# Performance work log

Measured on AMD Instinct MI355X. Metric: run time of the kernel, lower is better.

## Reference

```python
import jax, jax.numpy as jnp
import numpy as np

BS, SL, D, H = 8, 1024, 1024, 16
DK = D // H


def setup_inputs() -> dict:
    key = jax.random.key(0)
    ks = jax.random.split(key, 12)
    mk = lambda k, shape, s=1.0: jax.random.normal(k, shape, dtype=jnp.float32) * s
    return {
        "q": mk(ks[0], (BS, SL, D)),
        "k": mk(ks[1], (BS, SL, D)),
        "v": mk(ks[2], (BS, SL, D)),
        "mask": jax.random.randint(ks[3], (BS, SL), 0, 2, dtype=jnp.int32),
        "wq": mk(ks[4], (D, D), 0.02), "bq": jnp.zeros((D,), jnp.float32),
        "wk": mk(ks[5], (D, D), 0.02), "bk": jnp.zeros((D,), jnp.float32),
        "wv": mk(ks[6], (D, D), 0.02), "bv": jnp.zeros((D,), jnp.float32),
        "wo": mk(ks[7], (D, D), 0.02), "bo": jnp.zeros((D,), jnp.float32),
    }


def reference(q, k, v, mask, wq, bq, wk, bk, wv, bv, wo, bo):
    bs, sl, d = q.shape
    # linear projections (torch Linear: x @ W^T + b), split heads -> [b, h, s, dk]
    def proj(x, w, b):
        return (x @ w.T + b).reshape(bs, sl, H, DK).transpose(0, 2, 1, 3)
    qh, kh, vh = proj(q, wq, bq), proj(k, wk, bk), proj(v, wv, bv)
    # scaled scores [b, h, sq, sk]
    scores = jnp.einsum("bhqd,bhkd->bhqk", qh, kh) / jnp.sqrt(jnp.float32(DK))
    # mask query rows: mask [b, s] -> [b, 1, s, 1]
    m = mask[:, None, :, None]
    scores = jnp.where(m == 0, jnp.float32(-1e9), scores)
    # NOTE: original code computes transform(scores) but discards it; the output
    # path uses the raw masked/scaled scores (dropout is identity at eval).
    ctx = jnp.einsum("bhqk,bhkd->bhqd", scores, vh)  # [b, h, s, dk]
    concat = ctx.transpose(0, 2, 1, 3).reshape(bs, sl, d)
    return concat @ wo.T + bo
```

## Files before the change

kernel.cpp:

```cpp
#include <hip/hip_runtime.h>
#include <hip/hip_bf16.h>
#include <stdint.h>

#define BSZ 8
#define SLEN 1024
#define DMODEL 1024
#define NH 16
#define HD 64
#define MROWS (BSZ * SLEN)
#define NT 16

typedef __bf16 bf16_t;
typedef __bf16 bf16x8 __attribute__((ext_vector_type(8)));
typedef __bf16 bf16x4 __attribute__((ext_vector_type(4)));
typedef float f32x4 __attribute__((ext_vector_type(4)));

__device__ __forceinline__ void gload_lds16(const void* g, void* l) {
    __builtin_amdgcn_global_load_lds(
        (const __attribute__((address_space(1))) unsigned int*)g,
        (__attribute__((address_space(3))) unsigned int*)l, 16, 0, 0);
}

__global__ __launch_bounds__(256) void cvt3(
    const float* __restrict__ s0, const float* __restrict__ s1, const float* __restrict__ s2,
    bf16_t* __restrict__ o0, bf16_t* __restrict__ o1, bf16_t* __restrict__ o2, int n4) {
    const float* s = s0; bf16_t* d = o0;
    if (blockIdx.y == 1) { s = s1; d = o1; }
    else if (blockIdx.y == 2) { s = s2; d = o2; }
    int i = blockIdx.x * blockDim.x + threadIdx.x;
    if (i >= n4) return;
    const float4 v = reinterpret_cast<const float4*>(s)[i];
    bf16x4 o;
    o[0] = (bf16_t)v.x; o[1] = (bf16_t)v.y; o[2] = (bf16_t)v.z; o[3] = (bf16_t)v.w;
    reinterpret_cast<bf16x4*>(d)[i] = o;
}

__device__ __forceinline__ void mfma_quad(f32x4 (&acc)[8][4], int mb,
                                          const bf16x8 (&afr)[4], const bf16x8 (&bfr)[4]) {
    __builtin_amdgcn_s_setprio(1);
#pragma unroll
    for (int m = 0; m < 4; ++m)
#pragma unroll
        for (int n = 0; n < 4; ++n)
            acc[mb + m][n] = __builtin_amdgcn_mfma_f32_16x16x32_bf16(
                afr[m], bfr[n], acc[mb + m][n], 0, 0, 0);
    __builtin_amdgcn_s_setprio(0);
}

template <int FINAL>
__global__ __launch_bounds__(512, 2) void gemm256(
    const bf16_t* __restrict__ A0, const bf16_t* __restrict__ B0p, void* __restrict__ C0, const float* __restrict__ bias0,
    const bf16_t* __restrict__ A1, const bf16_t* __restrict__ B1p, void* __restrict__ C1, const float* __restrict__ bias1,
    const bf16_t* __restrict__ A2, const bf16_t* __restrict__ B2p, void* __restrict__ C2, const float* __restrict__ bias2,
    const float* __restrict__ trow, const int* __restrict__ mask) {
    __shared__ __align__(16) bf16_t As[4][256 * 32];
    __shared__ __align__(16) bf16_t Bs[4][256 * 32];
    const int tid = threadIdx.x;
    const int lane = tid & 63, wave = tid >> 6;
    const int wm = wave >> 2, wn = wave & 3;
    const int lr = lane & 15, g = lane >> 4;

    const bf16_t* A = A0; const bf16_t* B = B0p; void* C = C0; const float* bias = bias0;
    if (blockIdx.z == 1) { A = A1; B = B1p; C = C1; bias = bias1; }
    else if (blockIdx.z == 2) { A = A2; B = B2p; C = C2; bias = bias2; }

    const int m0 = blockIdx.y * 256;
    const int n0 = blockIdx.x * 256;
    if (FINAL) B += (size_t)(m0 >> 10) * SLEN * DMODEL;

    const int q0 = wave * 64 + lane, q1 = 512 + q0;
    const int row0 = q0 >> 2, row1 = q1 >> 2;
    const int gl0 = ((q0 & 3) - (row0 >> 1)) & 3;
    const int gl1 = ((q1 & 3) - (row1 >> 1)) & 3;
    const int sOfs0 = row0 * DMODEL + gl0 * 8;
    const int sOfs1 = row1 * DMODEL + gl1 * 8;
    const bf16_t* Ag = A + (size_t)m0 * DMODEL;
    const bf16_t* Bg = B + (size_t)n0 * DMODEL;
    char* const AsB = (char*)&As[0][0];
    char* const BsB = (char*)&Bs[0][0];
    const int d0 = q0 * 16, d1 = q1 * 16;

    int aoff[8], boff[4];
#pragma unroll
    for (int mi = 0; mi < 8; ++mi) {
        const int r = wm * 128 + mi * 16 + lr;
        aoff[mi] = r * 64 + (((g + (r >> 1)) & 3) << 4);
    }
#pragma unroll
    for (int ni = 0; ni < 4; ++ni) {
        const int r = wn * 64 + ni * 16 + lr;
        boff[ni] = r * 64 + (((g + (r >> 1)) & 3) << 4);
    }

    f32x4 acc[8][4] = {};

    gload_lds16(Ag + sOfs0, AsB + d0);
    gload_lds16(Ag + sOfs1, AsB + d1);
    gload_lds16(Bg + sOfs0, BsB + d0);
    gload_lds16(Bg + sOfs1, BsB + d1);
    gload_lds16(Ag + sOfs0 + 32, AsB + 16384 + d0);
    gload_lds16(Ag + sOfs1 + 32, AsB + 16384 + d1);
    gload_lds16(Bg + sOfs0 + 32, BsB + 16384 + d0);
    gload_lds16(Bg + sOfs1 + 32, BsB + 16384 + d1);

    for (int t = 0; t < NT; ++t) {
        const int cur = t & 1, nxt = cur ^ 1;
        const int kn = ((t + 1 < NT) ? (t + 1) : 0) * 64;
        const char* Ac0 = AsB + cur * 32768;
        const char* Ac1 = Ac0 + 16384;
        const char* Bc0 = BsB + cur * 32768;
        const char* Bc1 = Bc0 + 16384;
        char* An0 = AsB + nxt * 32768; char* An1 = An0 + 16384;
        char* Bn0 = BsB + nxt * 32768; char* Bn1 = Bn0 + 16384;
        bf16x8 afr[4], bfr[4];

        asm volatile("s_waitcnt vmcnt(4)" ::: "memory");
        __builtin_amdgcn_s_barrier();
        __builtin_amdgcn_sched_barrier(0);
        gload_lds16(Ag + sOfs0 + kn, An0 + d0);
        gload_lds16(Ag + sOfs1 + kn, An0 + d1);
#pragma unroll
        for (int i = 0; i < 4; ++i) bfr[i] = *reinterpret_cast<const bf16x8*>(Bc0 + boff[i]);
#pragma unroll
        for (int i = 0; i < 4; ++i) afr[i] = *reinterpret_cast<const bf16x8*>(Ac0 + aoff[i]);
        mfma_quad(acc, 0, afr, bfr);

        gload_lds16(Bg + sOfs0 + kn, Bn0 + d0);
        gload_lds16(Bg + sOfs1 + kn, Bn0 + d1);
#pragma unroll
        for (int i = 0; i < 4; ++i) afr[i] = *reinterpret_cast<const bf16x8*>(Ac0 + aoff[4 + i]);
        mfma_quad(acc, 4, afr, bfr);

        asm volatile("s_waitcnt vmcnt(4)" ::: "memory");
        __builtin_amdgcn_s_barrier();
        __builtin_amdgcn_sched_barrier(0);
        gload_lds16(Ag + sOfs0 + kn + 32, An1 + d0);
        gload_lds16(Ag + sOfs1 + kn + 32, An1 + d1);
#pragma unroll
        for (int i = 0; i < 4; ++i) bfr[i] = *reinterpret_cast<const bf16x8*>(Bc1 + boff[i]);
#pragma unroll
        for (int i = 0; i < 4; ++i) afr[i] = *reinterpret_cast<const bf16x8*>(Ac1 + aoff[i]);
        mfma_quad(acc, 0, afr, bfr);

        gload_lds16(Bg + sOfs0 + kn + 32, Bn1 + d0);
        gload_lds16(Bg + sOfs1 + kn + 32, Bn1 + d1);
#pragma unroll
        for (int i = 0; i < 4; ++i) afr[i] = *reinterpret_cast<const bf16x8*>(Ac1 + aoff[4 + i]);
        mfma_quad(acc, 4, afr, bfr);
    }

    const int lq4 = g * 4;
    if (FINAL == 0) {
        bf16_t* Co = (bf16_t*)C;
#pragma unroll
        for (int mi = 0; mi < 8; ++mi)
#pragma unroll
            for (int ni = 0; ni < 4; ++ni) {
                const int col = n0 + wn * 64 + ni * 16 + lr;
                const float bcol = bias[col];
#pragma unroll
                for (int r = 0; r < 4; ++r) {
                    const int row = m0 + wm * 128 + mi * 16 + lq4 + r;
                    Co[(size_t)row * DMODEL + col] = (bf16_t)(acc[mi][ni][r] + bcol);
                }
            }
    } else {
        float* Co = (float*)C;
#pragma unroll
        for (int mi = 0; mi < 8; ++mi)
#pragma unroll
            for (int ni = 0; ni < 4; ++ni) {
                const int col = n0 + wn * 64 + ni * 16 + lr;
                const float bcol = bias[col];
#pragma unroll
                for (int r = 0; r < 4; ++r) {
                    const int row = m0 + wm * 128 + mi * 16 + lq4 + r;
                    const int b = row >> 10, s = row & 1023;
                    float v;
                    if (mask[b * SLEN + s]) v = acc[mi][ni][r] * 0.125f + bcol;
                    else v = trow[(size_t)b * DMODEL + col];
                    Co[(size_t)row * DMODEL + col] = v;
                }
            }
    }
}

__global__ __launch_bounds__(512) void compute_w(
    const bf16_t* __restrict__ Kh, const bf16_t* __restrict__ Vh,
    float* __restrict__ Wpart) {
    __shared__ float Ksf[64 * 64];
    __shared__ float Vsf[64 * 64];
    const int h = blockIdx.x;
    const int b = blockIdx.y;
    const int ks = blockIdx.z;
    const int tid = threadIdx.x;
    const int dd = tid & 63;
    const int eg = tid >> 6;
    const int srow = tid >> 3;
    const int sseg = (tid & 7) * 8;

    float acc[8] = {};
    for (int kc = 0; kc < 8; ++kc) {
        const int kbase = ks * 512 + kc * 64;
        const size_t roff = (size_t)(b * SLEN + kbase + srow) * DMODEL + h * HD + sseg;
        bf16x8 kv = *reinterpret_cast<const bf16x8*>(&Kh[roff]);
        bf16x8 vv = *reinterpret_cast<const bf16x8*>(&Vh[roff]);
#pragma unroll
        for (int j = 0; j < 8; ++j) {
            Ksf[srow * 64 + sseg + j] = (float)kv[j];
            Vsf[srow * 64 + sseg + j] = (float)vv[j];
        }
        __syncthreads();
#pragma unroll 4
        for (int kk = 0; kk < 64; ++kk) {
            const float vval = Vsf[kk * 64 + dd];
#pragma unroll
            for (int i = 0; i < 8; ++i)
                acc[i] += Ksf[kk * 64 + eg * 8 + i] * vval;
        }
        __syncthreads();
    }
    float* Wo = Wpart + (((size_t)ks * BSZ + b) * NH + h) * 4096;
#pragma unroll
    for (int i = 0; i < 8; ++i)
        Wo[(eg * 8 + i) * 64 + dd] = acc[i];
}

__global__ __launch_bounds__(256) void colsum_v(
    const bf16_t* __restrict__ Vh, float* __restrict__ Spart) {
    const int dseg = blockIdx.x;
    const int b = blockIdx.y;
    const int ks = blockIdx.z;
    const int d = dseg * 256 + threadIdx.x;
    float acc = 0.f;
#pragma unroll 8
    for (int k = ks * 128; k < ks * 128 + 128; ++k)
        acc += (float)Vh[(size_t)(b * SLEN + k) * DMODEL + d];
    Spart[((size_t)ks * BSZ + b) * DMODEL + d] = acc;
}

__global__ __launch_bounds__(256) void compute_t(
    const float* __restrict__ Spart, const float* __restrict__ wo,
    const float* __restrict__ bo, float* __restrict__ t) {
    __shared__ float Ss[DMODEL];
    const int b = blockIdx.x >> 8;
    const int j0 = (blockIdx.x & 255) * 4;
    const int tid = threadIdx.x;
#pragma unroll
    for (int i = 0; i < 4; ++i) {
        const int d = i * 256 + tid;
        float s = 0.f;
#pragma unroll
        for (int ks = 0; ks < 8; ++ks) s += Spart[((size_t)ks * BSZ + b) * DMODEL + d];
        Ss[d] = s;
    }
    __syncthreads();
    const int wave = tid >> 6, lane = tid & 63;
    const int j = j0 + wave;
    f32x4 acc = {};
#pragma unroll
    for (int it = 0; it < 4; ++it) {
        const int idx = it * 256 + lane * 4;
        const f32x4 wv = *reinterpret_cast<const f32x4*>(&wo[(size_t)j * DMODEL + idx]);
        const f32x4 sv = *reinterpret_cast<const f32x4*>(&Ss[idx]);
        acc += wv * sv;
    }
    float tot = acc[0] + acc[1] + acc[2] + acc[3];
#pragma unroll
    for (int off = 1; off < 64; off <<= 1) tot += __shfl_xor(tot, off, 64);
    if (lane == 0) t[(size_t)b * DMODEL + j] = -1e9f * tot + bo[j];
}

__global__ __launch_bounds__(256) void compute_pt(
    const float* __restrict__ Wpart, const float* __restrict__ wo,
    bf16_t* __restrict__ PT) {
    __shared__ float Ws[64 * 65];
    __shared__ float Wos[128 * 64];
    const int jt = blockIdx.x;
    const int h = blockIdx.y;
    const int b = blockIdx.z;
    const int tid = threadIdx.x;
    const int j0 = jt * 128;
    const float* W0 = Wpart + (((size_t)0 * BSZ + b) * NH + h) * 4096;
    const float* W1 = Wpart + (((size_t)1 * BSZ + b) * NH + h) * 4096;
#pragma unroll
    for (int i = 0; i < 16; ++i) {
        const int idx = i * 256 + tid;
        Ws[(idx >> 6) * 65 + (idx & 63)] = W0[idx] + W1[idx];
    }
#pragma unroll
    for (int i = 0; i < 32; ++i) {
        const int idx = i * 256 + tid;
        Wos[idx] = wo[(size_t)(j0 + (idx >> 6)) * DMODEL + h * HD + (idx & 63)];
    }
    __syncthreads();
    const int e = tid & 63;
    const int jb = tid >> 6;
    for (int jj2 = 0; jj2 < 32; ++jj2) {
        const int jj = jb * 32 + jj2;
        float acc = 0.f;
#pragma unroll
        for (int dd = 0; dd < 64; ++dd)
            acc += Wos[jj * 64 + dd] * Ws[e * 65 + dd];
        PT[((size_t)b * SLEN + j0 + jj) * DMODEL + h * HD + e] = (bf16_t)acc;
    }
}

extern "C" void kernel_launch(void* const* d_in, const int* in_sizes, int n_in,
                              void* d_out, int out_size, void* d_ws, size_t ws_size,
                              hipStream_t stream) {
    const float* q  = (const float*)d_in[0];
    const float* k  = (const float*)d_in[1];
    const float* v  = (const float*)d_in[2];
    const int* mask = (const int*)d_in[3];
    const float* wq = (const float*)d_in[4];
    const float* bq = (const float*)d_in[5];
    const float* wk = (const float*)d_in[6];
    const float* bk = (const float*)d_in[7];
    const float* wv = (const float*)d_in[8];
    const float* bv = (const float*)d_in[9];
    const float* wo = (const float*)d_in[10];
    const float* bo = (const float*)d_in[11];

    char* ws = (char*)d_ws;
    const size_t SZ_ACT = (size_t)MROWS * DMODEL * 2;
    const size_t SZ_W = (size_t)DMODEL * DMODEL * 2;
    const size_t SZ_WPART = (size_t)2 * 8 * 16 * 4096 * 4;
    const size_t SZ_SPART = (size_t)8 * 8 * 1024 * 4;
    const size_t SZ_TROW = (size_t)8 * 1024 * 4;
    const size_t need_roomy = 6 * SZ_ACT + 3 * SZ_W + SZ_WPART + SZ_SPART + SZ_TROW;
    const bool roomy = ws_size >= need_roomy;

    bf16_t* qb = (bf16_t*)(ws);
    bf16_t* kb = (bf16_t*)(ws + SZ_ACT);
    bf16_t* vb = (bf16_t*)(ws + 2 * SZ_ACT);
    bf16_t* Qh = (bf16_t*)(ws + 3 * SZ_ACT);
    bf16_t *Kh, *Vh, *PT;
    char* tail;
    if (roomy) {
        Kh = (bf16_t*)(ws + 4 * SZ_ACT);
        Vh = (bf16_t*)(ws + 5 * SZ_ACT);
        PT = qb;
        tail = ws + 6 * SZ_ACT;
    } else {
        Kh = qb; Vh = kb; PT = vb;
        tail = ws + 4 * SZ_ACT;
    }
    bf16_t* wqb = (bf16_t*)(tail);
    bf16_t* wkb = (bf16_t*)(tail + SZ_W);
    bf16_t* wvb = (bf16_t*)(tail + 2 * SZ_W);
    float* Wpart = (float*)(tail + 3 * SZ_W);
    float* Spart = (float*)(tail + 3 * SZ_W + SZ_WPART);
    float* trow  = (float*)(tail + 3 * SZ_W + SZ_WPART + SZ_SPART);

    const int n4a = MROWS * DMODEL / 4;
    const int n4w = DMODEL * DMODEL / 4;
    cvt3<<<dim3(n4a / 256, 3), 256, 0, stream>>>(q, k, v, qb, kb, vb, n4a);
    cvt3<<<dim3(n4w / 256, 3), 256, 0, stream>>>(wq, wk, wv, wqb, wkb, wvb, n4w);

    if (roomy) {
        gemm256<0><<<dim3(4, 32, 3), 512, 0, stream>>>(
            qb, wqb, Qh, bq, kb, wkb, Kh, bk, vb, wvb, Vh, bv, nullptr, nullptr);
    } else {
        gemm256<0><<<dim3(4, 32, 1), 512, 0, stream>>>(
            qb, wqb, Qh, bq, qb, wqb, Qh, bq, qb, wqb, Qh, bq, nullptr, nullptr);
        gemm256<0><<<dim3(4, 32, 1), 512, 0, stream>>>(
            kb, wkb, Kh, bk, kb, wkb, Kh, bk, kb, wkb, Kh, bk, nullptr, nullptr);
        gemm256<0><<<dim3(4, 32, 1), 512, 0, stream>>>(
            vb, wvb, Vh, bv, vb, wvb, Vh, bv, vb, wvb, Vh, bv, nullptr, nullptr);
    }

    compute_w<<<dim3(NH, BSZ, 2), 512, 0, stream>>>(Kh, Vh, Wpart);
    colsum_v<<<dim3(4, BSZ, 8), 256, 0, stream>>>(Vh, Spart);
    compute_t<<<dim3(2048), 256, 0, stream>>>(Spart, wo, bo, trow);
    compute_pt<<<dim3(8, NH, BSZ), 256, 0, stream>>>(Wpart, wo, PT);

    gemm256<1><<<dim3(4, 32, 1), 512, 0, stream>>>(
        Qh, PT, d_out, bo, Qh, PT, d_out, bo, Qh, PT, d_out, bo, trow, mask);
}
```

Measured before the change: 350.9 us.

## Restructure GEMMs to 256x128 tiles, transpose K/V projections, MFMA-based W and PT kernels

The GEMM tile becomes 256x128 with a 1D swizzled grid covering all three projection slices. K and V projections are computed transposed (weights times activations) so the per-head K^T V product can be done with MFMA in a new wker kernel, which also produces V column sums. compute_pt is replaced by an MFMA kernel over bf16 Wo, and all seven input conversions are merged into one launch. This cuts scalar FP32 work and launch count. In exchange it always needs a large workspace (the low-memory fallback is removed) and adds more bf16 rounding of intermediates.

```diff
diff --git a/kernel.cpp b/kernel.cpp
--- a/kernel.cpp
+++ b/kernel.cpp
@@ -2,12 +2,12 @@
 #include <hip/hip_bf16.h>
 #include <stdint.h>
 
-#define BSZ 8
+#define BATCH 8
 #define SLEN 1024
 #define DMODEL 1024
 #define NH 16
 #define HD 64
-#define MROWS (BSZ * SLEN)
+#define MROWS (BATCH * SLEN)
 #define NT 16
 
 typedef __bf16 bf16_t;
@@ -21,226 +21,268 @@
         (__attribute__((address_space(3))) unsigned int*)l, 16, 0, 0);
 }
 
-__global__ __launch_bounds__(256) void cvt3(
+__global__ __launch_bounds__(256) void cvt7(
     const float* __restrict__ s0, const float* __restrict__ s1, const float* __restrict__ s2,
-    bf16_t* __restrict__ o0, bf16_t* __restrict__ o1, bf16_t* __restrict__ o2, int n4) {
-    const float* s = s0; bf16_t* d = o0;
-    if (blockIdx.y == 1) { s = s1; d = o1; }
-    else if (blockIdx.y == 2) { s = s2; d = o2; }
+    const float* __restrict__ s3, const float* __restrict__ s4, const float* __restrict__ s5,
+    const float* __restrict__ s6,
+    bf16_t* __restrict__ o0, bf16_t* __restrict__ o1, bf16_t* __restrict__ o2,
+    bf16_t* __restrict__ o3, bf16_t* __restrict__ o4, bf16_t* __restrict__ o5,
+    bf16_t* __restrict__ o6, int n4a, int n4w) {
+    const float* srcs[7] = {s0, s1, s2, s3, s4, s5, s6};
+    bf16_t* dsts[7] = {o0, o1, o2, o3, o4, o5, o6};
+    const int y = blockIdx.y;
+    const int n4 = (y < 3) ? n4a : n4w;
     int i = blockIdx.x * blockDim.x + threadIdx.x;
     if (i >= n4) return;
-    const float4 v = reinterpret_cast<const float4*>(s)[i];
+    const float4 v = reinterpret_cast<const float4*>(srcs[y])[i];
     bf16x4 o;
     o[0] = (bf16_t)v.x; o[1] = (bf16_t)v.y; o[2] = (bf16_t)v.z; o[3] = (bf16_t)v.w;
-    reinterpret_cast<bf16x4*>(d)[i] = o;
-}
-
-__device__ __forceinline__ void mfma_quad(f32x4 (&acc)[8][4], int mb,
-                                          const bf16x8 (&afr)[4], const bf16x8 (&bfr)[4]) {
+    reinterpret_cast<bf16x4*>(dsts[y])[i] = o;
+}
+
+struct Slice {
+    const bf16_t* A; const bf16_t* B; void* C; const float* bias; int M, N, brow;
+};
+
+#define AHALF 16384
+#define BHALF 8192
+
+__device__ __forceinline__ void mfma8(f32x4 (&acc)[8][2], int mb,
+                                      const bf16x8 (&afr)[4], const bf16x8 (&bfr)[2]) {
     __builtin_amdgcn_s_setprio(1);
 #pragma unroll
     for (int m = 0; m < 4; ++m)
 #pragma unroll
-        for (int n = 0; n < 4; ++n)
+        for (int n = 0; n < 2; ++n)
             acc[mb + m][n] = __builtin_amdgcn_mfma_f32_16x16x32_bf16(
                 afr[m], bfr[n], acc[mb + m][n], 0, 0, 0);
     __builtin_amdgcn_s_setprio(0);
 }
 
 template <int FINAL>
-__global__ __launch_bounds__(512, 2) void gemm256(
-    const bf16_t* __restrict__ A0, const bf16_t* __restrict__ B0p, void* __restrict__ C0, const float* __restrict__ bias0,
-    const bf16_t* __restrict__ A1, const bf16_t* __restrict__ B1p, void* __restrict__ C1, const float* __restrict__ bias1,
-    const bf16_t* __restrict__ A2, const bf16_t* __restrict__ B2p, void* __restrict__ C2, const float* __restrict__ bias2,
+__global__ __launch_bounds__(512, 2) void gemm_tiled(
+    Slice s0, Slice s1, Slice s2,
     const float* __restrict__ trow, const int* __restrict__ mask) {
-    __shared__ __align__(16) bf16_t As[4][256 * 32];
-    __shared__ __align__(16) bf16_t Bs[4][256 * 32];
+    __shared__ __align__(16) char As[4 * AHALF];
+    __shared__ __align__(16) char Bs[4 * BHALF];
     const int tid = threadIdx.x;
     const int lane = tid & 63, wave = tid >> 6;
     const int wm = wave >> 2, wn = wave & 3;
     const int lr = lane & 15, g = lane >> 4;
 
-    const bf16_t* A = A0; const bf16_t* B = B0p; void* C = C0; const float* bias = bias0;
-    if (blockIdx.z == 1) { A = A1; B = B1p; C = C1; bias = bias1; }
-    else if (blockIdx.z == 2) { A = A2; B = B2p; C = C2; bias = bias2; }
-
-    const int m0 = blockIdx.y * 256;
-    const int n0 = blockIdx.x * 256;
+    const int nb = gridDim.x;
+    const int bid = blockIdx.x;
+    const int swz = (bid & 7) * (nb >> 3) + (bid >> 3);
+    const int sl = swz >> 8;
+    const int w = swz & 255;
+    Slice S = (sl == 0) ? s0 : (sl == 1) ? s1 : s2;
+    const int ntn = S.N >> 7;
+    const int ty = w / ntn, tx = w - ty * ntn;
+    const int m0 = ty * 256, n0 = tx * 128;
+    const bf16_t* A = S.A;
+    const bf16_t* B = S.B;
     if (FINAL) B += (size_t)(m0 >> 10) * SLEN * DMODEL;
 
-    const int q0 = wave * 64 + lane, q1 = 512 + q0;
-    const int row0 = q0 >> 2, row1 = q1 >> 2;
-    const int gl0 = ((q0 & 3) - (row0 >> 1)) & 3;
-    const int gl1 = ((q1 & 3) - (row1 >> 1)) & 3;
-    const int sOfs0 = row0 * DMODEL + gl0 * 8;
-    const int sOfs1 = row1 * DMODEL + gl1 * 8;
-    const bf16_t* Ag = A + (size_t)m0 * DMODEL;
-    const bf16_t* Bg = B + (size_t)n0 * DMODEL;
-    char* const AsB = (char*)&As[0][0];
-    char* const BsB = (char*)&Bs[0][0];
-    const int d0 = q0 * 16, d1 = q1 * 16;
-
-    int aoff[8], boff[4];
+    const int qa0 = tid, qa1 = tid + 512, qb = tid;
+    const int rA0 = qa0 >> 2, rA1 = qa1 >> 2, rB = qb >> 2;
+    const int glA0 = ((qa0 & 3) - (rA0 >> 1)) & 3;
+    const int glA1 = ((qa1 & 3) - (rA1 >> 1)) & 3;
+    const int glB  = ((qb  & 3) - (rB  >> 1)) & 3;
+    const bf16_t* Ag0 = A + (size_t)(m0 + rA0) * DMODEL + glA0 * 8;
+    const bf16_t* Ag1 = A + (size_t)(m0 + rA1) * DMODEL + glA1 * 8;
+    const bf16_t* Bg  = B + (size_t)(n0 + rB)  * DMODEL + glB  * 8;
+    const int dA0 = qa0 * 16, dA1 = qa1 * 16, dB = qb * 16;
+
+    int aoff[8], boff[2];
 #pragma unroll
     for (int mi = 0; mi < 8; ++mi) {
         const int r = wm * 128 + mi * 16 + lr;
         aoff[mi] = r * 64 + (((g + (r >> 1)) & 3) << 4);
     }
 #pragma unroll
-    for (int ni = 0; ni < 4; ++ni) {
-        const int r = wn * 64 + ni * 16 + lr;
+    for (int ni = 0; ni < 2; ++ni) {
+        const int r = wn * 32 + ni * 16 + lr;
         boff[ni] = r * 64 + (((g + (r >> 1)) & 3) << 4);
     }
 
-    f32x4 acc[8][4] = {};
-
-    gload_lds16(Ag + sOfs0, AsB + d0);
-    gload_lds16(Ag + sOfs1, AsB + d1);
-    gload_lds16(Bg + sOfs0, BsB + d0);
-    gload_lds16(Bg + sOfs1, BsB + d1);
-    gload_lds16(Ag + sOfs0 + 32, AsB + 16384 + d0);
-    gload_lds16(Ag + sOfs1 + 32, AsB + 16384 + d1);
-    gload_lds16(Bg + sOfs0 + 32, BsB + 16384 + d0);
-    gload_lds16(Bg + sOfs1 + 32, BsB + 16384 + d1);
+    f32x4 acc[8][2] = {};
+
+    gload_lds16(Ag0, As + dA0);
+    gload_lds16(Ag1, As + dA1);
+    gload_lds16(Bg,  Bs + dB);
+    gload_lds16(Ag0 + 32, As + AHALF + dA0);
+    gload_lds16(Ag1 + 32, As + AHALF + dA1);
+    gload_lds16(Bg  + 32, Bs + BHALF + dB);
 
     for (int t = 0; t < NT; ++t) {
         const int cur = t & 1, nxt = cur ^ 1;
         const int kn = ((t + 1 < NT) ? (t + 1) : 0) * 64;
-        const char* Ac0 = AsB + cur * 32768;
-        const char* Ac1 = Ac0 + 16384;
-        const char* Bc0 = BsB + cur * 32768;
-        const char* Bc1 = Bc0 + 16384;
-        char* An0 = AsB + nxt * 32768; char* An1 = An0 + 16384;
-        char* Bn0 = BsB + nxt * 32768; char* Bn1 = Bn0 + 16384;
-        bf16x8 afr[4], bfr[4];
-
-        asm volatile("s_waitcnt vmcnt(4)" ::: "memory");
+        const char* Ac0 = As + cur * 2 * AHALF;
+        const char* Ac1 = Ac0 + AHALF;
+        const char* Bc0 = Bs + cur * 2 * BHALF;
+        const char* Bc1 = Bc0 + BHALF;
+        char* An0 = As + nxt * 2 * AHALF; char* An1 = An0 + AHALF;
+        char* Bn0 = Bs + nxt * 2 * BHALF; char* Bn1 = Bn0 + BHALF;
+        bf16x8 afr[4], bfr[2];
+
+        asm volatile("s_waitcnt vmcnt(3)" ::: "memory");
         __builtin_amdgcn_s_barrier();
         __builtin_amdgcn_sched_barrier(0);
-        gload_lds16(Ag + sOfs0 + kn, An0 + d0);
-        gload_lds16(Ag + sOfs1 + kn, An0 + d1);
-#pragma unroll
-        for (int i = 0; i < 4; ++i) bfr[i] = *reinterpret_cast<const bf16x8*>(Bc0 + boff[i]);
+        gload_lds16(Ag0 + kn, An0 + dA0);
+        gload_lds16(Ag1 + kn, An0 + dA1);
+#pragma unroll
+        for (int i = 0; i < 2; ++i) bfr[i] = *reinterpret_cast<const bf16x8*>(Bc0 + boff[i]);
 #pragma unroll
         for (int i = 0; i < 4; ++i) afr[i] = *reinterpret_cast<const bf16x8*>(Ac0 + aoff[i]);
-        mfma_quad(acc, 0, afr, bfr);
-
-        gload_lds16(Bg + sOfs0 + kn, Bn0 + d0);
-        gload_lds16(Bg + sOfs1 + kn, Bn0 + d1);
+        mfma8(acc, 0, afr, bfr);
+
+        gload_lds16(Bg + kn, Bn0 + dB);
 #pragma unroll
         for (int i = 0; i < 4; ++i) afr[i] = *reinterpret_cast<const bf16x8*>(Ac0 + aoff[4 + i]);
-        mfma_quad(acc, 4, afr, bfr);
-
-        asm volatile("s_waitcnt vmcnt(4)" ::: "memory");
+        mfma8(acc, 4, afr, bfr);
+
+        asm volatile("s_waitcnt vmcnt(3)" ::: "memory");
         __builtin_amdgcn_s_barrier();
         __builtin_amdgcn_sched_barrier(0);
-        gload_lds16(Ag + sOfs0 + kn + 32, An1 + d0);
-        gload_lds16(Ag + sOfs1 + kn + 32, An1 + d1);
-#pragma unroll
-        for (int i = 0; i < 4; ++i) bfr[i] = *reinterpret_cast<const bf16x8*>(Bc1 + boff[i]);
+        gload_lds16(Ag0 + kn + 32, An1 + dA0);
+        gload_lds16(Ag1 + kn + 32, An1 + dA1);
+#pragma unroll
+        for (int i = 0; i < 2; ++i) bfr[i] = *reinterpret_cast<const bf16x8*>(Bc1 + boff[i]);
 #pragma unroll
         for (int i = 0; i < 4; ++i) afr[i] = *reinterpret_cast<const bf16x8*>(Ac1 + aoff[i]);
-        mfma_quad(acc, 0, afr, bfr);
-
-        gload_lds16(Bg + sOfs0 + kn + 32, Bn1 + d0);
-        gload_lds16(Bg + sOfs1 + kn + 32, Bn1 + d1);
+        mfma8(acc, 0, afr, bfr);
+
+        gload_lds16(Bg + kn + 32, Bn1 + dB);
 #pragma unroll
         for (int i = 0; i < 4; ++i) afr[i] = *reinterpret_cast<const bf16x8*>(Ac1 + aoff[4 + i]);
-        mfma_quad(acc, 4, afr, bfr);
-    }
-
-    const int lq4 = g * 4;
+        mfma8(acc, 4, afr, bfr);
+    }
+
+    const int N = S.N;
     if (FINAL == 0) {
-        bf16_t* Co = (bf16_t*)C;
+        bf16_t* Co = (bf16_t*)S.C;
 #pragma unroll
         for (int mi = 0; mi < 8; ++mi)
 #pragma unroll
-            for (int ni = 0; ni < 4; ++ni) {
-                const int col = n0 + wn * 64 + ni * 16 + lr;
-                const float bcol = bias[col];
+            for (int ni = 0; ni < 2; ++ni) {
+                const int col = n0 + wn * 32 + ni * 16 + lr;
 #pragma unroll
                 for (int r = 0; r < 4; ++r) {
-                    const int row = m0 + wm * 128 + mi * 16 + lq4 + r;
-                    Co[(size_t)row * DMODEL + col] = (bf16_t)(acc[mi][ni][r] + bcol);
+                    const int row = m0 + wm * 128 + mi * 16 + g * 4 + r;
+                    const float bv = S.bias[S.brow ? row : col];
+                    Co[(size_t)row * N + col] = (bf16_t)(acc[mi][ni][r] + bv);
                 }
             }
     } else {
-        float* Co = (float*)C;
+        float* Co = (float*)S.C;
 #pragma unroll
         for (int mi = 0; mi < 8; ++mi)
 #pragma unroll
-            for (int ni = 0; ni < 4; ++ni) {
-                const int col = n0 + wn * 64 + ni * 16 + lr;
-                const float bcol = bias[col];
+            for (int ni = 0; ni < 2; ++ni) {
+                const int col = n0 + wn * 32 + ni * 16 + lr;
+                const float bcol = S.bias[col];
 #pragma unroll
                 for (int r = 0; r < 4; ++r) {
-                    const int row = m0 + wm * 128 + mi * 16 + lq4 + r;
+                    const int row = m0 + wm * 128 + mi * 16 + g * 4 + r;
                     const int b = row >> 10, s = row & 1023;
-                    float v;
-                    if (mask[b * SLEN + s]) v = acc[mi][ni][r] * 0.125f + bcol;
-                    else v = trow[(size_t)b * DMODEL + col];
-                    Co[(size_t)row * DMODEL + col] = v;
+                    float vv;
+                    if (mask[b * SLEN + s]) vv = acc[mi][ni][r] * 0.125f + bcol;
+                    else vv = trow[(size_t)b * DMODEL + col];
+                    Co[(size_t)row * N + col] = vv;
                 }
             }
     }
 }
 
-__global__ __launch_bounds__(512) void compute_w(
-    const bf16_t* __restrict__ Kh, const bf16_t* __restrict__ Vh,
-    float* __restrict__ Wpart) {
-    __shared__ float Ksf[64 * 64];
-    __shared__ float Vsf[64 * 64];
-    const int h = blockIdx.x;
-    const int b = blockIdx.y;
-    const int ks = blockIdx.z;
+__global__ __launch_bounds__(256) void wker(
+    const bf16_t* __restrict__ KhT, const bf16_t* __restrict__ VhT,
+    bf16_t* __restrict__ Wb, float* __restrict__ Svec) {
+    __shared__ __align__(16) char Ka[2][16384];
+    __shared__ __align__(16) char Va[2][16384];
+    __shared__ float red[64 * 16];
+    const int h = blockIdx.x, b = blockIdx.y;
     const int tid = threadIdx.x;
-    const int dd = tid & 63;
-    const int eg = tid >> 6;
-    const int srow = tid >> 3;
-    const int sseg = (tid & 7) * 8;
-
-    float acc[8] = {};
-    for (int kc = 0; kc < 8; ++kc) {
-        const int kbase = ks * 512 + kc * 64;
-        const size_t roff = (size_t)(b * SLEN + kbase + srow) * DMODEL + h * HD + sseg;
-        bf16x8 kv = *reinterpret_cast<const bf16x8*>(&Kh[roff]);
-        bf16x8 vv = *reinterpret_cast<const bf16x8*>(&Vh[roff]);
-#pragma unroll
-        for (int j = 0; j < 8; ++j) {
-            Ksf[srow * 64 + sseg + j] = (float)kv[j];
-            Vsf[srow * 64 + sseg + j] = (float)vv[j];
+    const int lane = tid & 63, wave = tid >> 6;
+    const int lr = lane & 15, g = lane >> 4;
+
+    int srcOfs[4], dstOfs[4];
+#pragma unroll
+    for (int c = 0; c < 4; ++c) {
+        const int gq = c * 256 + tid;
+        const int row = gq >> 4, slot = gq & 15;
+        const int gl = (slot - row) & 15;
+        srcOfs[c] = row * MROWS + gl * 8;
+        dstOfs[c] = gq * 16;
+    }
+    const bf16_t* Kg = KhT + (size_t)(h * HD) * MROWS + b * SLEN;
+    const bf16_t* Vg = VhT + (size_t)(h * HD) * MROWS + b * SLEN;
+
+    f32x4 acc[4] = {};
+    float svp[4] = {};
+
+#pragma unroll
+    for (int c = 0; c < 4; ++c) gload_lds16(Kg + srcOfs[c], Ka[0] + dstOfs[c]);
+#pragma unroll
+    for (int c = 0; c < 4; ++c) gload_lds16(Vg + srcOfs[c], Va[0] + dstOfs[c]);
+
+    for (int kt = 0; kt < 8; ++kt) {
+        const int cur = kt & 1;
+        if (kt < 7) {
+            const int ko = (kt + 1) * 128;
+#pragma unroll
+            for (int c = 0; c < 4; ++c) gload_lds16(Kg + ko + srcOfs[c], Ka[cur ^ 1] + dstOfs[c]);
+#pragma unroll
+            for (int c = 0; c < 4; ++c) gload_lds16(Vg + ko + srcOfs[c], Va[cur ^ 1] + dstOfs[c]);
         }
         __syncthreads();
-#pragma unroll 4
-        for (int kk = 0; kk < 64; ++kk) {
-            const float vval = Vsf[kk * 64 + dd];
-#pragma unroll
-            for (int i = 0; i < 8; ++i)
-                acc[i] += Ksf[kk * 64 + eg * 8 + i] * vval;
+        bf16x8 afr, bfr;
+        __builtin_amdgcn_s_setprio(1);
+#pragma unroll
+        for (int k4 = 0; k4 < 4; ++k4) {
+            const int ra = wave * 16 + lr;
+            afr = *reinterpret_cast<const bf16x8*>(Ka[cur] + ra * 256 + (((k4 * 4 + g + ra) & 15) << 4));
+#pragma unroll
+            for (int ni = 0; ni < 4; ++ni) {
+                const int rb = ni * 16 + lr;
+                bfr = *reinterpret_cast<const bf16x8*>(Va[cur] + rb * 256 + (((k4 * 4 + g + rb) & 15) << 4));
+                acc[ni] = __builtin_amdgcn_mfma_f32_16x16x32_bf16(afr, bfr, acc[ni], 0, 0, 0);
+            }
+        }
+        __builtin_amdgcn_s_setprio(0);
+#pragma unroll
+        for (int c = 0; c < 4; ++c) {
+            const bf16x8 vv = *reinterpret_cast<const bf16x8*>(Va[cur] + dstOfs[c]);
+#pragma unroll
+            for (int j = 0; j < 8; ++j) svp[c] += (float)vv[j];
         }
         __syncthreads();
     }
-    float* Wo = Wpart + (((size_t)ks * BSZ + b) * NH + h) * 4096;
-#pragma unroll
-    for (int i = 0; i < 8; ++i)
-        Wo[(eg * 8 + i) * 64 + dd] = acc[i];
-}
-
-__global__ __launch_bounds__(256) void colsum_v(
-    const bf16_t* __restrict__ Vh, float* __restrict__ Spart) {
-    const int dseg = blockIdx.x;
-    const int b = blockIdx.y;
-    const int ks = blockIdx.z;
-    const int d = dseg * 256 + threadIdx.x;
-    float acc = 0.f;
-#pragma unroll 8
-    for (int k = ks * 128; k < ks * 128 + 128; ++k)
-        acc += (float)Vh[(size_t)(b * SLEN + k) * DMODEL + d];
-    Spart[((size_t)ks * BSZ + b) * DMODEL + d] = acc;
+
+#pragma unroll
+    for (int c = 0; c < 4; ++c) red[(c * 16 + (tid >> 4)) * 16 + (tid & 15)] = svp[c];
+    __syncthreads();
+    if (tid < 64) {
+        float s = 0.f;
+#pragma unroll
+        for (int i = 0; i < 16; ++i) s += red[tid * 16 + i];
+        Svec[(size_t)b * DMODEL + h * HD + tid] = s;
+    }
+
+    bf16_t* Wo = Wb + ((size_t)(b * NH + h)) * 4096;
+#pragma unroll
+    for (int ni = 0; ni < 4; ++ni)
+#pragma unroll
+        for (int r = 0; r < 4; ++r) {
+            const int e = wave * 16 + g * 4 + r;
+            const int dd = ni * 16 + lr;
+            const int half = dd >> 5, gg = (dd & 31) >> 3, j = dd & 7;
+            const int idx = half * 2048 + e * 32 + (((gg + (e >> 1)) & 3) << 3) + j;
+            Wo[idx] = (bf16_t)acc[ni][r];
+        }
 }
 
 __global__ __launch_bounds__(256) void compute_t(
-    const float* __restrict__ Spart, const float* __restrict__ wo,
+    const float* __restrict__ Svec, const float* __restrict__ wo,
     const float* __restrict__ bo, float* __restrict__ t) {
     __shared__ float Ss[DMODEL];
     const int b = blockIdx.x >> 8;
@@ -249,10 +291,7 @@
 #pragma unroll
     for (int i = 0; i < 4; ++i) {
         const int d = i * 256 + tid;
-        float s = 0.f;
-#pragma unroll
-        for (int ks = 0; ks < 8; ++ks) s += Spart[((size_t)ks * BSZ + b) * DMODEL + d];
-        Ss[d] = s;
+        Ss[d] = Svec[(size_t)b * DMODEL + d];
     }
     __syncthreads();
     const int wave = tid >> 6, lane = tid & 63;
@@ -271,38 +310,68 @@
     if (lane == 0) t[(size_t)b * DMODEL + j] = -1e9f * tot + bo[j];
 }
 
-__global__ __launch_bounds__(256) void compute_pt(
-    const float* __restrict__ Wpart, const float* __restrict__ wo,
+__global__ __launch_bounds__(256) void ptker(
+    const bf16_t* __restrict__ wob, const bf16_t* __restrict__ Wb,
     bf16_t* __restrict__ PT) {
-    __shared__ float Ws[64 * 65];
-    __shared__ float Wos[128 * 64];
-    const int jt = blockIdx.x;
-    const int h = blockIdx.y;
-    const int b = blockIdx.z;
+    __shared__ __align__(16) char Wimg[8192];
+    __shared__ __align__(16) char Wo2[2][2][4096];
+    const int jt = blockIdx.x, h = blockIdx.y, b = blockIdx.z;
     const int tid = threadIdx.x;
-    const int j0 = jt * 128;
-    const float* W0 = Wpart + (((size_t)0 * BSZ + b) * NH + h) * 4096;
-    const float* W1 = Wpart + (((size_t)1 * BSZ + b) * NH + h) * 4096;
-#pragma unroll
-    for (int i = 0; i < 16; ++i) {
-        const int idx = i * 256 + tid;
-        Ws[(idx >> 6) * 65 + (idx & 63)] = W0[idx] + W1[idx];
-    }
-#pragma unroll
-    for (int i = 0; i < 32; ++i) {
-        const int idx = i * 256 + tid;
-        Wos[idx] = wo[(size_t)(j0 + (idx >> 6)) * DMODEL + h * HD + (idx & 63)];
-    }
+    const int lane = tid & 63, wave = tid >> 6;
+    const int lr = lane & 15, g = lane >> 4;
+
+    const bf16_t* Wsrc = Wb + ((size_t)(b * NH + h)) * 4096;
+    gload_lds16(Wsrc + tid * 8, Wimg + tid * 16);
+    gload_lds16(Wsrc + 2048 + tid * 8, Wimg + 4096 + tid * 16);
+
+    const int q = tid;
+    const int row = q >> 2, slot = q & 3;
+    const int gl = (slot - (row >> 1)) & 3;
+    const int jbase = jt * 512;
+    const bf16_t* wg = wob + (size_t)(jbase + row) * DMODEL + h * HD + gl * 8;
+    gload_lds16(wg,      Wo2[0][0] + q * 16);
+    gload_lds16(wg + 32, Wo2[0][1] + q * 16);
     __syncthreads();
-    const int e = tid & 63;
-    const int jb = tid >> 6;
-    for (int jj2 = 0; jj2 < 32; ++jj2) {
-        const int jj = jb * 32 + jj2;
-        float acc = 0.f;
-#pragma unroll
-        for (int dd = 0; dd < 64; ++dd)
-            acc += Wos[jj * 64 + dd] * Ws[e * 65 + dd];
-        PT[((size_t)b * SLEN + j0 + jj) * DMODEL + h * HD + e] = (bf16_t)acc;
+
+    bf16x8 bfr[2][4];
+#pragma unroll
+    for (int kh = 0; kh < 2; ++kh)
+#pragma unroll
+        for (int ni = 0; ni < 4; ++ni) {
+            const int e = ni * 16 + lr;
+            bfr[kh][ni] = *reinterpret_cast<const bf16x8*>(
+                Wimg + kh * 4096 + e * 64 + (((g + (e >> 1)) & 3) << 4));
+        }
+
+    for (int it = 0; it < 8; ++it) {
+        const int cur = it & 1;
+        if (it < 7) {
+            const bf16_t* wn = wg + (size_t)(it + 1) * 64 * DMODEL;
+            gload_lds16(wn,      Wo2[cur ^ 1][0] + q * 16);
+            gload_lds16(wn + 32, Wo2[cur ^ 1][1] + q * 16);
+        }
+        const int ra = wave * 16 + lr;
+        const int ao = ra * 64 + (((g + (ra >> 1)) & 3) << 4);
+        f32x4 acc[4] = {};
+        bf16x8 afr;
+        __builtin_amdgcn_s_setprio(1);
+#pragma unroll
+        for (int kh = 0; kh < 2; ++kh) {
+            afr = *reinterpret_cast<const bf16x8*>(Wo2[cur][kh] + ao);
+#pragma unroll
+            for (int ni = 0; ni < 4; ++ni)
+                acc[ni] = __builtin_amdgcn_mfma_f32_16x16x32_bf16(afr, bfr[kh][ni], acc[ni], 0, 0, 0);
+        }
+        __builtin_amdgcn_s_setprio(0);
+        bf16_t* Po = PT + (size_t)b * SLEN * DMODEL;
+#pragma unroll
+        for (int ni = 0; ni < 4; ++ni)
+#pragma unroll
+            for (int r = 0; r < 4; ++r) {
+                const int j = jbase + it * 64 + wave * 16 + g * 4 + r;
+                Po[(size_t)j * DMODEL + h * HD + ni * 16 + lr] = (bf16_t)acc[ni][r];
+            }
+        __syncthreads();
     }
 }
 
@@ -325,56 +394,37 @@
     char* ws = (char*)d_ws;
     const size_t SZ_ACT = (size_t)MROWS * DMODEL * 2;
     const size_t SZ_W = (size_t)DMODEL * DMODEL * 2;
-    const size_t SZ_WPART = (size_t)2 * 8 * 16 * 4096 * 4;
-    const size_t SZ_SPART = (size_t)8 * 8 * 1024 * 4;
-    const size_t SZ_TROW = (size_t)8 * 1024 * 4;
-    const size_t need_roomy = 6 * SZ_ACT + 3 * SZ_W + SZ_WPART + SZ_SPART + SZ_TROW;
-    const bool roomy = ws_size >= need_roomy;
-
-    bf16_t* qb = (bf16_t*)(ws);
-    bf16_t* kb = (bf16_t*)(ws + SZ_ACT);
-    bf16_t* vb = (bf16_t*)(ws + 2 * SZ_ACT);
-    bf16_t* Qh = (bf16_t*)(ws + 3 * SZ_ACT);
-    bf16_t *Kh, *Vh, *PT;
-    char* tail;
-    if (roomy) {
-        Kh = (bf16_t*)(ws + 4 * SZ_ACT);
-        Vh = (bf16_t*)(ws + 5 * SZ_ACT);
-        PT = qb;
-        tail = ws + 6 * SZ_ACT;
-    } else {
-        Kh = qb; Vh = kb; PT = vb;
-        tail = ws + 4 * SZ_ACT;
-    }
+    const size_t SZ_WB = (size_t)0x100000;
+    bf16_t* qb  = (bf16_t*)(ws);
+    bf16_t* kb  = (bf16_t*)(ws + SZ_ACT);
+    bf16_t* vb  = (bf16_t*)(ws + 2 * SZ_ACT);
+    bf16_t* Qh  = (bf16_t*)(ws + 3 * SZ_ACT);
+    bf16_t* KhT = (bf16_t*)(ws + 4 * SZ_ACT);
+    bf16_t* VhT = (bf16_t*)(ws + 5 * SZ_ACT);
+    char* tail = ws + 6 * SZ_ACT;
     bf16_t* wqb = (bf16_t*)(tail);
     bf16_t* wkb = (bf16_t*)(tail + SZ_W);
     bf16_t* wvb = (bf16_t*)(tail + 2 * SZ_W);
-    float* Wpart = (float*)(tail + 3 * SZ_W);
-    float* Spart = (float*)(tail + 3 * SZ_W + SZ_WPART);
-    float* trow  = (float*)(tail + 3 * SZ_W + SZ_WPART + SZ_SPART);
+    bf16_t* wob = (bf16_t*)(tail + 3 * SZ_W);
+    bf16_t* Wb  = (bf16_t*)(tail + 4 * SZ_W);
+    float* Svec = (float*)(tail + 4 * SZ_W + SZ_WB);
+    float* trow = (float*)(tail + 4 * SZ_W + SZ_WB + (size_t)(BATCH * DMODEL * 4));
+    bf16_t* PT  = qb;
 
     const int n4a = MROWS * DMODEL / 4;
     const int n4w = DMODEL * DMODEL / 4;
-    cvt3<<<dim3(n4a / 256, 3), 256, 0, stream>>>(q, k, v, qb, kb, vb, n4a);
-    cvt3<<<dim3(n4w / 256, 3), 256, 0, stream>>>(wq, wk, wv, wqb, wkb, wvb, n4w);
-
-    if (roomy) {
-        gemm256<0><<<dim3(4, 32, 3), 512, 0, stream>>>(
-            qb, wqb, Qh, bq, kb, wkb, Kh, bk, vb, wvb, Vh, bv, nullptr, nullptr);
-    } else {
-        gemm256<0><<<dim3(4, 32, 1), 512, 0, stream>>>(
-            qb, wqb, Qh, bq, qb, wqb, Qh, bq, qb, wqb, Qh, bq, nullptr, nullptr);
-        gemm256<0><<<dim3(4, 32, 1), 512, 0, stream>>>(
-            kb, wkb, Kh, bk, kb, wkb, Kh, bk, kb, wkb, Kh, bk, nullptr, nullptr);
-        gemm256<0><<<dim3(4, 32, 1), 512, 0, stream>>>(
-            vb, wvb, Vh, bv, vb, wvb, Vh, bv, vb, wvb, Vh, bv, nullptr, nullptr);
-    }
-
-    compute_w<<<dim3(NH, BSZ, 2), 512, 0, stream>>>(Kh, Vh, Wpart);
-    colsum_v<<<dim3(4, BSZ, 8), 256, 0, stream>>>(Vh, Spart);
-    compute_t<<<dim3(2048), 256, 0, stream>>>(Spart, wo, bo, trow);
-    compute_pt<<<dim3(8, NH, BSZ), 256, 0, stream>>>(Wpart, wo, PT);
-
-    gemm256<1><<<dim3(4, 32, 1), 512, 0, stream>>>(
-        Qh, PT, d_out, bo, Qh, PT, d_out, bo, Qh, PT, d_out, bo, trow, mask);
-}
+    cvt7<<<dim3(n4a / 256, 7), 256, 0, stream>>>(q, k, v, wq, wk, wv, wo,
+                                                 qb, kb, vb, wqb, wkb, wvb, wob, n4a, n4w);
+
+    Slice sq{qb,  wqb, Qh,  bq, MROWS,  DMODEL, 0};
+    Slice sk{wkb, kb,  KhT, bk, DMODEL, MROWS,  1};
+    Slice sv{wvb, vb,  VhT, bv, DMODEL, MROWS,  1};
+    gemm_tiled<0><<<dim3(768), 512, 0, stream>>>(sq, sk, sv, nullptr, nullptr);
+
+    wker<<<dim3(NH, BATCH), 256, 0, stream>>>(KhT, VhT, Wb, Svec);
+    compute_t<<<dim3(2048), 256, 0, stream>>>(Svec, wo, bo, trow);
+    ptker<<<dim3(2, NH, BATCH), 256, 0, stream>>>(wob, Wb, PT);
+
+    Slice so{Qh, PT, d_out, bo, MROWS, DMODEL, 0};
+    gemm_tiled<1><<<dim3(256), 512, 0, stream>>>(so, so, so, trow, mask);
+}
```

New measurement: 316.0 us. 9.9% less time.
